# Performance work log

Hardware: AMD Instinct MI355X
Metric: run time of the kernel (lower is better)

Reference implementation:

```python
import jax, jax.numpy as jnp
import numpy as np

# Static config (matches init_kwargs)
N = 1024        # node_num
F = 64          # input_dim (window length)
D = 64          # dim == embed_dim (heads=1)
TOPK = 20
B = 64
EPS = 1e-5      # BatchNorm eps
NEG_SLOPE = 0.2 # GraphLayer leaky_relu slope


def setup_inputs() -> dict:
    key = jax.random.key(0)
    ks = jax.random.split(key, 12)
    s = lambda fan: 1.0 / np.sqrt(fan)
    inp = {
        'data': jax.random.normal(ks[0], (B, N, F), jnp.float32),
        'org_edge_index': jax.random.randint(ks[1], (2, 2048), 0, N),
        'embedding': jax.random.normal(ks[2], (N, D), jnp.float32) * s(D),   # nn.Embedding(node_num, dim), xavier-ish
        'lin_w': jax.random.normal(ks[3], (F, D), jnp.float32) * s(F),       # GraphLayer lin (bias=False)
        'att_i': jax.random.normal(ks[4], (D,), jnp.float32) * s(D),
        'att_j': jax.random.normal(ks[5], (D,), jnp.float32) * s(D),
        'att_em_i': jax.random.normal(ks[6], (D,), jnp.float32) * s(D),
        'att_em_j': jax.random.normal(ks[7], (D,), jnp.float32) * s(D),
        'gnn_bias': jnp.zeros((D,), jnp.float32),
        'bn1_gamma': jnp.ones((D,), jnp.float32),  # GNNLayer.bn
        'bn1_beta': jnp.zeros((D,), jnp.float32),
        'bn2_gamma': jnp.ones((D,), jnp.float32),  # bn_outlayer_in
        'bn2_beta': jnp.zeros((D,), jnp.float32),
        'out_w': jax.random.normal(ks[8], (D, 1), jnp.float32) * s(D),       # OutLayer Linear(dim, 1)
        'out_b': jnp.zeros((1,), jnp.float32),
    }
    return inp


def _batchnorm(x, gamma, beta, axes):
    # training-mode BatchNorm: batch statistics over `axes`, per-feature affine
    mu = jnp.mean(x, axis=axes, keepdims=True)
    var = jnp.var(x, axis=axes, keepdims=True)
    return gamma * (x - mu) * jax.lax.rsqrt(var + EPS) + beta


def reference(data, org_edge_index, embedding, lin_w, att_i, att_j, att_em_i,
              att_em_j, gnn_bias, bn1_gamma, bn1_beta, bn2_gamma, bn2_beta,
              out_w, out_b):
    # --- dynamic graph construction from embedding cosine similarity ---
    w = jax.lax.stop_gradient(embedding)          # weights_arr.detach()
    nrm = jnp.linalg.norm(w, axis=-1)
    cos = (w @ w.T) / jnp.clip(nrm[:, None] * nrm[None, :], 1e-10)
    _, topi = jax.lax.top_k(cos, TOPK)            # [N, TOPK] neighbors j of each target i
    # (torch code drops edges whose cos value is exactly 0 -- measure-zero with
    #  random embeddings; edge count stays N*TOPK. Self edge i->i is always in topk,
    #  matching remove_self_loops + add_self_loops.)

    # --- GraphLayer (GAT-style, heads=1, concat=False, aggr='add') ---
    xl = jnp.einsum('bnf,fd->bnd', data, lin_w)   # linear transform, [B,N,D]
    xj = xl[:, topi]                               # gather neighbor feats [B,N,TOPK,D]
    ej = embedding[topi]                           # neighbor embeddings [N,TOPK,D]
    # alpha = <key_i, att_i||att_em_i> + <key_j, att_j||att_em_j>
    score = (xl @ att_i)[:, :, None] \
          + (embedding @ att_em_i)[None, :, None] \
          + jnp.einsum('bnkd,d->bnk', xj, att_j) \
          + (ej @ att_em_j)[None]                  # [B,N,TOPK]
    alpha = jax.nn.softmax(jax.nn.leaky_relu(score, NEG_SLOPE), axis=-1)
    gnn = jnp.einsum('bnk,bnkd->bnd', alpha, xj) + gnn_bias

    # GNNLayer.bn: BatchNorm1d over B*N samples, D channels
    gnn = _batchnorm(gnn, bn1_gamma, bn1_beta, axes=(0, 1))

    # --- readout ---
    out = gnn * embedding[None]                    # mul with node embedding
    out = jax.nn.relu(_batchnorm(out, bn2_gamma, bn2_beta, axes=(0, 1)))
    # dropout(0.2) -> identity (eval)
    pred = (out @ out_w + out_b).reshape(B, N)     # OutLayer: Linear(D, 1)
    return pred, out
```

## Files before the change

kernel.cpp:

```cpp
#include <hip/hip_runtime.h>

#define NN 1024
#define KK 20
#define BN 65536
#define NEG_SLOPE 0.2f

typedef unsigned short u16;
typedef unsigned int u32;
typedef unsigned long long u64;
typedef __attribute__((ext_vector_type(8))) short bf8;
typedef __attribute__((ext_vector_type(4))) float f32x4;

__device__ __forceinline__ float bf2f(u16 h) {
    return __uint_as_float(((u32)h) << 16);
}
__device__ __forceinline__ u16 f2bf(float f) {
    u32 u = __float_as_uint(f);
    u32 lsb = (u >> 16) & 1u;
    u += 0x7fffu + lsb;
    return (u16)(u >> 16);
}
__device__ __forceinline__ void up2(u32 w, float& a, float& b) {
    a = __uint_as_float(w << 16);
    b = __uint_as_float(w & 0xffff0000u);
}
__device__ __forceinline__ bool is_bf(const void* g1) {
    return *(const u32*)g1 == 0x3F803F80u;
}
template <bool BF>
__device__ __forceinline__ float ldf(const void* p, size_t i) {
    if (BF) return bf2f(((const u16*)p)[i]);
    return ((const float*)p)[i];
}
template <bool BF>
__device__ __forceinline__ void stf(void* p, size_t i, float v) {
    if (BF) ((u16*)p)[i] = f2bf(v);
    else ((float*)p)[i] = v;
}
template <bool BF>
__device__ __forceinline__ void ldf2(const void* p, size_t pairidx, float& a, float& b) {
    if (BF) {
        u32 w = ((const u32*)p)[pairidx];
        up2(w, a, b);
    } else {
        float2 v = ((const float2*)p)[pairidx];
        a = v.x;
        b = v.y;
    }
}

template <bool BF>
__device__ void k1a_body(const void* emb, const void* aei, const void* aej,
                         u16* nwH, u16* nwL, float* e_i, float* e_j, float* stats) {
    __shared__ float sme[4][64], sm2[4][64];
    int tid = threadIdx.x;
    int lane = tid & 63, wave = tid >> 6;
    int n = blockIdx.x * 4 + wave;
    float v = ldf<BF>(emb, n * 64 + lane);
    sme[wave][lane] = v;
    sm2[wave][lane] = v * v;
    float s2 = v * v;
    float si = v * ldf<BF>(aei, lane);
    float sj = v * ldf<BF>(aej, lane);
#pragma unroll
    for (int off = 32; off; off >>= 1) {
        s2 += __shfl_xor(s2, off, 64);
        si += __shfl_xor(si, off, 64);
        sj += __shfl_xor(sj, off, 64);
    }
    float rq = rsqrtf(fmaxf(s2, 1e-20f));
    float x = v * rq;
    u16 h = f2bf(x);
    nwH[n * 64 + lane] = h;
    nwL[n * 64 + lane] = f2bf(x - bf2f(h));
    if (lane == 0) { e_i[n] = si; e_j[n] = sj; }
    __syncthreads();
    if (tid < 64) {
        float u1 = sme[0][tid] + sme[1][tid] + sme[2][tid] + sme[3][tid];
        atomicAdd(&stats[320 + tid], 64.f * u1);
    } else if (tid < 128) {
        int d = tid - 64;
        float u2 = sm2[0][d] + sm2[1][d] + sm2[2][d] + sm2[3][d];
        atomicAdd(&stats[384 + d], 64.f * u2);
    }
}
__global__ __launch_bounds__(256) void k1a_norm(const void* emb, const void* aei, const void* aej,
                                                const void* probe, u16* nwH, u16* nwL,
                                                float* e_i, float* e_j, float* stats) {
    if (is_bf(probe)) k1a_body<true>(emb, aei, aej, nwH, nwL, e_i, e_j, stats);
    else k1a_body<false>(emb, aei, aej, nwH, nwL, e_i, e_j, stats);
}

__global__ __launch_bounds__(256) void k1b_gram(const u16* __restrict__ nwH,
                                                const u16* __restrict__ nwL,
                                                float* __restrict__ G) {
    int tid = threadIdx.x;
    int lane = tid & 63, wave = tid >> 6;
    int c = lane & 15, quad = lane >> 4;
    int rowblk = blockIdx.x >> 4, colblk = blockIdx.x & 15;
    int arow = rowblk * 64 + wave * 16 + c;
    bf8 aH[2], aL[2];
#pragma unroll
    for (int s = 0; s < 2; ++s) {
        aH[s] = *(const bf8*)(nwH + (size_t)arow * 64 + s * 32 + quad * 8);
        aL[s] = *(const bf8*)(nwL + (size_t)arow * 64 + s * 32 + quad * 8);
    }
    f32x4 acc[4] = {{0.f, 0.f, 0.f, 0.f}, {0.f, 0.f, 0.f, 0.f}, {0.f, 0.f, 0.f, 0.f}, {0.f, 0.f, 0.f, 0.f}};
#pragma unroll
    for (int t = 0; t < 4; ++t) {
        int bnode = colblk * 64 + t * 16 + c;
#pragma unroll
        for (int s = 0; s < 2; ++s) {
            bf8 bH = *(const bf8*)(nwH + (size_t)bnode * 64 + s * 32 + quad * 8);
            bf8 bL = *(const bf8*)(nwL + (size_t)bnode * 64 + s * 32 + quad * 8);
            acc[t] = __builtin_amdgcn_mfma_f32_16x16x32_bf16(aH[s], bH, acc[t], 0, 0, 0);
            acc[t] = __builtin_amdgcn_mfma_f32_16x16x32_bf16(aH[s], bL, acc[t], 0, 0, 0);
            acc[t] = __builtin_amdgcn_mfma_f32_16x16x32_bf16(aL[s], bH, acc[t], 0, 0, 0);
        }
    }
#pragma unroll
    for (int t = 0; t < 4; ++t) {
#pragma unroll
        for (int reg = 0; reg < 4; ++reg) {
            int row = rowblk * 64 + wave * 16 + quad * 4 + reg;
            G[(size_t)row * 1024 + colblk * 64 + t * 16 + c] = acc[t][reg];
        }
    }
}

__global__ __launch_bounds__(256) void k1c_select(const float* __restrict__ G, int* __restrict__ topi) {
    int lane = threadIdx.x & 63, wave = threadIdx.x >> 6;
    int n = blockIdx.x * 4 + wave;
    const f32x4* gp = (const f32x4*)(G + (size_t)n * 1024 + lane * 16);
    f32x4 v0 = gp[0], v1 = gp[1], v2 = gp[2], v3 = gp[3];
    float c[16] = {v0.x, v0.y, v0.z, v0.w, v1.x, v1.y, v1.z, v1.w,
                   v2.x, v2.y, v2.z, v2.w, v3.x, v3.y, v3.z, v3.w};
    u32 o[16];
#pragma unroll
    for (int j = 0; j < 16; ++j) {
        u32 u = __float_as_uint(c[j]);
        o[j] = u ^ (u32)(((int)u >> 31) | 0x80000000);
    }
    unsigned mask = 0u;
    int keep = 0;
    for (int r = 0; r < KK; ++r) {
        u32 bo = 0u;
        int bj = 0;
#pragma unroll
        for (int j = 0; j < 16; ++j) {
            bool t = !((mask >> j) & 1u) && o[j] > bo;
            bo = t ? o[j] : bo;
            bj = t ? j : bj;
        }
        u64 key = ((u64)bo << 32) | (u32)(~(u32)(lane * 16 + bj));
#pragma unroll
        for (int off = 32; off; off >>= 1) {
            u64 ok = __shfl_xor((unsigned long long)key, off, 64);
            key = ok > key ? ok : key;
        }
        int bm = (int)((~(u32)key) & 1023u);
        if ((bm >> 4) == lane) mask |= 1u << (bm & 15);
        if (lane == r) keep = bm;
    }
    if (lane < KK) topi[n * KK + lane] = keep;
}

template <bool BF>
__device__ void k2_body(const void* data, const void* lin_w, const void* att_i, const void* att_j,
                        u16* xl, float* a_i, float* a_j) {
    __shared__ u16 Bl[64 * 72];
    __shared__ u16 Ct[64 * 72];
    int tid = threadIdx.x;
    {
        int k = tid >> 2, n0 = (tid & 3) * 16;
        if (BF) {
            const u16* lw = (const u16*)lin_w;
#pragma unroll
            for (int i = 0; i < 16; ++i) Bl[(n0 + i) * 72 + k] = lw[k * 64 + n0 + i];
        } else {
            const float* lw = (const float*)lin_w;
#pragma unroll
            for (int i = 0; i < 16; ++i) Bl[(n0 + i) * 72 + k] = f2bf(lw[k * 64 + n0 + i]);
        }
    }
    __syncthreads();
    int lane = tid & 63, wave = tid >> 6;
    int c = lane & 15, quad = lane >> 4;
    int m0 = blockIdx.x * 64 + wave * 16;
    size_t row = (size_t)(m0 + c);
    f32x4 acc[4] = {{0.f, 0.f, 0.f, 0.f}, {0.f, 0.f, 0.f, 0.f}, {0.f, 0.f, 0.f, 0.f}, {0.f, 0.f, 0.f, 0.f}};
#pragma unroll
    for (int s = 0; s < 2; ++s) {
        bf8 a;
        if (BF) {
            a = *(const bf8*)((const u16*)data + row * 64 + s * 32 + quad * 8);
        } else {
            const float* dp = (const float*)data + row * 64 + s * 32 + quad * 8;
            f32x4 x0 = *(const f32x4*)dp;
            f32x4 x1 = *(const f32x4*)(dp + 4);
            a[0] = (short)f2bf(x0.x); a[1] = (short)f2bf(x0.y);
            a[2] = (short)f2bf(x0.z); a[3] = (short)f2bf(x0.w);
            a[4] = (short)f2bf(x1.x); a[5] = (short)f2bf(x1.y);
            a[6] = (short)f2bf(x1.z); a[7] = (short)f2bf(x1.w);
        }
#pragma unroll
        for (int t = 0; t < 4; ++t) {
            bf8 b = *(const bf8*)&Bl[(t * 16 + c) * 72 + s * 32 + quad * 8];
            acc[t] = __builtin_amdgcn_mfma_f32_16x16x32_bf16(a, b, acc[t], 0, 0, 0);
        }
    }
    float wi[4], wj[4];
#pragma unroll
    for (int t = 0; t < 4; ++t) {
        wi[t] = ldf<BF>(att_i, t * 16 + c);
        wj[t] = ldf<BF>(att_j, t * 16 + c);
    }
    float ai4[4] = {0.f, 0.f, 0.f, 0.f}, aj4[4] = {0.f, 0.f, 0.f, 0.f};
#pragma unroll
    for (int t = 0; t < 4; ++t) {
#pragma unroll
        for (int reg = 0; reg < 4; ++reg) {
            float v = acc[t][reg];
            Ct[(wave * 16 + quad * 4 + reg) * 72 + t * 16 + c] = f2bf(v);
            ai4[reg] += v * wi[t];
            aj4[reg] += v * wj[t];
        }
    }
#pragma unroll
    for (int reg = 0; reg < 4; ++reg) {
#pragma unroll
        for (int off = 1; off < 16; off <<= 1) {
            ai4[reg] += __shfl_xor(ai4[reg], off, 64);
            aj4[reg] += __shfl_xor(aj4[reg], off, 64);
        }
    }
    if (c == 0) {
#pragma unroll
        for (int reg = 0; reg < 4; ++reg) {
            a_i[m0 + quad * 4 + reg] = ai4[reg];
            a_j[m0 + quad * 4 + reg] = aj4[reg];
        }
    }
    __syncthreads();
    {
        int r = tid >> 2, seg = tid & 3;
        uint4 v0 = *(const uint4*)&Ct[r * 72 + seg * 16];
        uint4 v1 = *(const uint4*)&Ct[r * 72 + seg * 16 + 8];
        uint4* dst = (uint4*)xl + ((size_t)(blockIdx.x * 64 + r) * 8 + seg * 2);
        dst[0] = v0;
        dst[1] = v1;
    }
}
__global__ __launch_bounds__(256) void k2_mfma(const void* data, const void* lin_w,
                                               const void* att_i, const void* att_j, const void* probe,
                                               u16* xl, float* a_i, float* a_j) {
    if (is_bf(probe)) k2_body<true>(data, lin_w, att_i, att_j, xl, a_i, a_j);
    else k2_body<false>(data, lin_w, att_i, att_j, xl, a_i, a_j);
}

template <bool BF>
__device__ void k3_body(const u16* xl, const int* topi, const float* a_i, const float* a_j,
                        const float* e_i, const float* e_j, const void* emb,
                        const void* gnn_bias, void* dout, float* stats) {
    extern __shared__ char smem[];
    u32* slice = (u32*)smem;
    float* aje = (float*)(smem + 131072);
    float* aie = (float*)(smem + 135168);
    uint2* sp = (uint2*)(smem + 136192);
    int tid = threadIdx.x;
    int b = blockIdx.x & 63;
    int q = blockIdx.x >> 6;
    int n0 = q * 256;
    const uint4* src = (const uint4*)(xl + ((size_t)b << 16));
    uint4* dst = (uint4*)slice;
#pragma unroll
    for (int r = 0; r < 8; ++r) dst[r * 1024 + tid] = src[r * 1024 + tid];
    aje[tid] = a_j[(b << 10) + tid] + e_j[tid];
    if (tid < 256) aie[tid] = a_i[(b << 10) + n0 + tid] + e_i[n0 + tid];
    __syncthreads();
    int lane = tid & 63, wave = tid >> 6;
    int half = lane >> 5, hl = lane & 31;
    int hwid = wave * 2 + half;
    float bias0, bias1;
    ldf2<BF>(gnn_bias, hl, bias0, bias1);
    float se[10];
#pragma unroll
    for (int s = 0; s < 10; ++s) se[s] = 0.f;
    int nl0 = hwid * 8;
    int t = (hl < KK) ? topi[(n0 + nl0) * KK + hl] : 0;
    for (int ii = 0; ii < 8; ++ii) {
        int nl = nl0 + ii;
        int n = n0 + nl;
        int pair = (b << 10) + n;
        int tc = t;
        if (ii < 7 && hl < KK) t = topi[(n + 1) * KK + hl];
        float sc = -3e38f;
        if (hl < KK) {
            sc = aie[nl] + aje[tc];
            sc = sc >= 0.f ? sc : NEG_SLOPE * sc;
        }
        float m = sc;
#pragma unroll
        for (int off = 16; off; off >>= 1) m = fmaxf(m, __shfl_xor(m, off, 32));
        float p = (hl < KK) ? __expf(sc - m) : 0.f;
        float S = p;
#pragma unroll
        for (int off = 16; off; off >>= 1) S += __shfl_xor(S, off, 32);
        if (hl < KK) {
            uint2 v; v.x = (u32)tc; v.y = __float_as_uint(p / S);
            sp[hwid * KK + hl] = v;
        }
        float acc0 = 0.f, acc1 = 0.f;
#pragma unroll
        for (int k = 0; k < KK; ++k) {
            uint2 v = sp[hwid * KK + k];
            u32 w = slice[(v.x << 5) + hl];
            float alpha = __uint_as_float(v.y);
            acc0 += alpha * __uint_as_float(w << 16);
            acc1 += alpha * __uint_as_float(w & 0xffff0000u);
        }
        acc0 += bias0;
        acc1 += bias1;
        if (BF) {
            u32 pk = (u32)f2bf(acc0) | ((u32)f2bf(acc1) << 16);
            ((u32*)dout)[(BN >> 1) + pair * 32 + hl] = pk;
        } else {
            float2 v2; v2.x = acc0; v2.y = acc1;
            ((float2*)dout)[(BN >> 1) + pair * 32 + hl] = v2;
        }
        float em0, em1;
        ldf2<BF>(emb, n * 32 + hl, em0, em1);
        se[0] += acc0; se[1] += acc1;
        se[2] += acc0 * acc0; se[3] += acc1 * acc1;
        float ge0 = acc0 * em0, ge1 = acc1 * em1;
        se[4] += ge0; se[5] += ge1;
        se[6] += ge0 * ge0; se[7] += ge1 * ge1;
        se[8] += ge0 * em0; se[9] += ge1 * em1;
    }
#pragma unroll
    for (int s = 0; s < 10; ++s) se[s] += __shfl_xor(se[s], 32, 64);
    __syncthreads();
    float* ps = (float*)smem;
    if (half == 0) {
#pragma unroll
        for (int s = 0; s < 5; ++s) {
            ps[wave * 320 + s * 64 + 2 * hl] = se[2 * s];
            ps[wave * 320 + s * 64 + 2 * hl + 1] = se[2 * s + 1];
        }
    }
    __syncthreads();
    if (tid < 320) {
        float s = 0.f;
#pragma unroll
        for (int w = 0; w < 16; ++w) s += ps[w * 320 + tid];
        atomicAdd(&stats[tid], s);
    }
}
__global__ __launch_bounds__(1024) void k3_gnn(const u16* xl, const int* topi, const float* a_i,
                                               const float* a_j, const float* e_i, const float* e_j,
                                               const void* emb, const void* gnn_bias, const void* probe,
                                               void* dout, float* stats) {
    if (is_bf(probe)) k3_body<true>(xl, topi, a_i, a_j, e_i, e_j, emb, gnn_bias, dout, stats);
    else k3_body<false>(xl, topi, a_i, a_j, e_i, e_j, emb, gnn_bias, dout, stats);
}

template <bool BF>
__device__ void k5_body(const void* emb, const float* stats, const void* g1, const void* b1,
                        const void* g2, const void* b2, const void* out_w, const void* out_b,
                        void* dout) {
    int lane = threadIdx.x & 63;
    float P, Q, R;
    {
        int d = lane;
        double inv = 1.0 / 65536.0;
        double S1 = stats[d], S2 = stats[64 + d], T1 = stats[128 + d], T2 = stats[192 + d];
        double T3 = stats[256 + d], U1 = stats[320 + d], U2 = stats[384 + d];
        double mu1 = S1 * inv;
        double var1 = S2 * inv - mu1 * mu1;
        if (var1 < 0.0) var1 = 0.0;
        double r1 = 1.0 / sqrt(var1 + 1e-5);
        double A = (double)ldf<BF>(g1, d) * r1;
        double C = (double)ldf<BF>(b1, d) - A * mu1;
        double E1 = A * T1 + C * U1;
        double mu2 = E1 * inv;
        double E2 = A * A * T2 + 2.0 * A * C * T3 + C * C * U2;
        double var2 = E2 * inv - mu2 * mu2;
        if (var2 < 0.0) var2 = 0.0;
        double r2 = 1.0 / sqrt(var2 + 1e-5);
        double g2r2 = (double)ldf<BF>(g2, d) * r2;
        P = (float)(g2r2 * A);
        Q = (float)(g2r2 * C);
        R = (float)((double)ldf<BF>(b2, d) - g2r2 * mu2);
    }
    int gw = (blockIdx.x * 256 + threadIdx.x) >> 6;
    float wo = ldf<BF>(out_w, lane);
    float ob = ldf<BF>(out_b, 0);
    int row0 = gw * 8;
    for (int i = 0; i < 8; ++i) {
        int row = row0 + i;
        int n = row & 1023;
        size_t oi = (size_t)BN + (size_t)row * 64 + lane;
        float g = ldf<BF>(dout, oi);
        float em = ldf<BF>(emb, n * 64 + lane);
        float o = fmaxf(P * g * em + Q * em + R, 0.f);
        stf<BF>(dout, oi, o);
        float p = o * wo;
#pragma unroll
        for (int off = 32; off; off >>= 1) p += __shfl_xor(p, off, 64);
        if (lane == 0) stf<BF>(dout, row, p + ob);
    }
}
__global__ __launch_bounds__(256) void k5_out(const void* emb, const float* stats, const void* g1,
                                              const void* b1, const void* g2, const void* b2,
                                              const void* out_w, const void* out_b, void* dout) {
    if (is_bf(g1)) k5_body<true>(emb, stats, g1, b1, g2, b2, out_w, out_b, dout);
    else k5_body<false>(emb, stats, g1, b1, g2, b2, out_w, out_b, dout);
}

extern "C" void kernel_launch(void* const* d_in, const int* in_sizes, int n_in,
                              void* d_out, int out_size, void* d_ws, size_t ws_size,
                              hipStream_t stream) {
    const void* data = d_in[0];
    const void* emb = d_in[2];
    const void* lin_w = d_in[3];
    const void* att_i = d_in[4];
    const void* att_j = d_in[5];
    const void* att_em_i = d_in[6];
    const void* att_em_j = d_in[7];
    const void* gnn_bias = d_in[8];
    const void* bn1_g = d_in[9];
    const void* bn1_b = d_in[10];
    const void* bn2_g = d_in[11];
    const void* bn2_b = d_in[12];
    const void* out_w = d_in[13];
    const void* out_b = d_in[14];

    char* ws = (char*)d_ws;
    float* a_i = (float*)ws;
    float* a_j = a_i + 65536;
    float* e_i = a_j + 65536;
    float* e_j = e_i + 1024;
    float* stats = e_j + 1024;
    int* topi = (int*)(stats + 448);
    u16* xl = (u16*)(topi + 20480);
    u16* nwH = xl + 4194304;
    u16* nwL = nwH + 65536;
    float* G = (float*)(nwL + 65536);

    hipMemsetAsync(stats, 0, 448 * sizeof(float), stream);
    k1a_norm<<<256, 256, 0, stream>>>(emb, att_em_i, att_em_j, bn1_g, nwH, nwL, e_i, e_j, stats);
    k1b_gram<<<256, 256, 0, stream>>>(nwH, nwL, G);
    k1c_select<<<256, 256, 0, stream>>>(G, topi);
    k2_mfma<<<1024, 256, 0, stream>>>(data, lin_w, att_i, att_j, bn1_g, xl, a_i, a_j);
    k3_gnn<<<256, 1024, 141312, stream>>>(xl, topi, a_i, a_j, e_i, e_j, emb, gnn_bias, bn1_g,
                                          d_out, stats);
    k5_out<<<2048, 256, 0, stream>>>(emb, stats, bn1_g, bn1_b, bn2_g, bn2_b, out_w, out_b, d_out);
}
```

Baseline: 164.9 us.

## Merge top-k select into xl GEMM launch and software-pipeline attention softmax

```diff
diff --git a/kernel.cpp b/kernel.cpp
--- a/kernel.cpp
+++ b/kernel.cpp
@@ -128,9 +128,9 @@
     }
 }
 
-__global__ __launch_bounds__(256) void k1c_select(const float* __restrict__ G, int* __restrict__ topi) {
+__device__ void k1c_body(int blk, const float* __restrict__ G, int* __restrict__ topi) {
     int lane = threadIdx.x & 63, wave = threadIdx.x >> 6;
-    int n = blockIdx.x * 4 + wave;
+    int n = blk * 4 + wave;
     const f32x4* gp = (const f32x4*)(G + (size_t)n * 1024 + lane * 16);
     f32x4 v0 = gp[0], v1 = gp[1], v2 = gp[2], v3 = gp[3];
     float c[16] = {v0.x, v0.y, v0.z, v0.w, v1.x, v1.y, v1.z, v1.w,
@@ -166,8 +166,8 @@
 }
 
 template <bool BF>
-__device__ void k2_body(const void* data, const void* lin_w, const void* att_i, const void* att_j,
-                        u16* xl, float* a_i, float* a_j) {
+__device__ void k2_body(int blk, const void* data, const void* lin_w, const void* att_i,
+                        const void* att_j, u16* xl, float* a_i, float* a_j) {
     __shared__ u16 Bl[64 * 72];
     __shared__ u16 Ct[64 * 72];
     int tid = threadIdx.x;
@@ -186,7 +186,7 @@
     __syncthreads();
     int lane = tid & 63, wave = tid >> 6;
     int c = lane & 15, quad = lane >> 4;
-    int m0 = blockIdx.x * 64 + wave * 16;
+    int m0 = blk * 64 + wave * 16;
     size_t row = (size_t)(m0 + c);
     f32x4 acc[4] = {{0.f, 0.f, 0.f, 0.f}, {0.f, 0.f, 0.f, 0.f}, {0.f, 0.f, 0.f, 0.f}, {0.f, 0.f, 0.f, 0.f}};
 #pragma unroll
@@ -246,16 +246,22 @@
         int r = tid >> 2, seg = tid & 3;
         uint4 v0 = *(const uint4*)&Ct[r * 72 + seg * 16];
         uint4 v1 = *(const uint4*)&Ct[r * 72 + seg * 16 + 8];
-        uint4* dst = (uint4*)xl + ((size_t)(blockIdx.x * 64 + r) * 8 + seg * 2);
+        uint4* dst = (uint4*)xl + ((size_t)(blk * 64 + r) * 8 + seg * 2);
         dst[0] = v0;
         dst[1] = v1;
     }
 }
-__global__ __launch_bounds__(256) void k2_mfma(const void* data, const void* lin_w,
-                                               const void* att_i, const void* att_j, const void* probe,
-                                               u16* xl, float* a_i, float* a_j) {
-    if (is_bf(probe)) k2_body<true>(data, lin_w, att_i, att_j, xl, a_i, a_j);
-    else k2_body<false>(data, lin_w, att_i, att_j, xl, a_i, a_j);
+
+__global__ __launch_bounds__(256) void k12_fused(const void* data, const void* lin_w,
+                                                 const void* att_i, const void* att_j,
+                                                 const void* probe, u16* xl, float* a_i,
+                                                 float* a_j, const float* G, int* topi) {
+    if (blockIdx.x < 1024) {
+        if (is_bf(probe)) k2_body<true>(blockIdx.x, data, lin_w, att_i, att_j, xl, a_i, a_j);
+        else k2_body<false>(blockIdx.x, data, lin_w, att_i, att_j, xl, a_i, a_j);
+    } else {
+        k1c_body(blockIdx.x - 1024, G, topi);
+    }
 }
 
 template <bool BF>
@@ -287,40 +293,68 @@
 #pragma unroll
     for (int s = 0; s < 10; ++s) se[s] = 0.f;
     int nl0 = hwid * 8;
-    int t = (hl < KK) ? topi[(n0 + nl0) * KK + hl] : 0;
+    u32 tc = 0;
+    float al = 0.f;
+    {
+        int t = (hl < KK) ? topi[(n0 + nl0) * KK + hl] : 0;
+        float sc = -3e38f;
+        if (hl < KK) {
+            sc = aie[nl0] + aje[t];
+            sc = sc >= 0.f ? sc : NEG_SLOPE * sc;
+        }
+        float m = sc;
+#pragma unroll
+        for (int off = 16; off; off >>= 1) m = fmaxf(m, __shfl_xor(m, off, 32));
+        float p = (hl < KK) ? __expf(sc - m) : 0.f;
+        float S = p;
+#pragma unroll
+        for (int off = 16; off; off >>= 1) S += __shfl_xor(S, off, 32);
+        tc = (u32)t;
+        al = p / S;
+    }
     for (int ii = 0; ii < 8; ++ii) {
         int nl = nl0 + ii;
         int n = n0 + nl;
         int pair = (b << 10) + n;
-        int tc = t;
-        if (ii < 7 && hl < KK) t = topi[(n + 1) * KK + hl];
-        float sc = -3e38f;
         if (hl < KK) {
-            sc = aie[nl] + aje[tc];
-            sc = sc >= 0.f ? sc : NEG_SLOPE * sc;
-        }
-        float m = sc;
-#pragma unroll
-        for (int off = 16; off; off >>= 1) m = fmaxf(m, __shfl_xor(m, off, 32));
-        float p = (hl < KK) ? __expf(sc - m) : 0.f;
-        float S = p;
-#pragma unroll
-        for (int off = 16; off; off >>= 1) S += __shfl_xor(S, off, 32);
-        if (hl < KK) {
-            uint2 v; v.x = (u32)tc; v.y = __float_as_uint(p / S);
+            uint2 v; v.x = tc; v.y = __float_as_uint(al);
             sp[hwid * KK + hl] = v;
         }
-        float acc0 = 0.f, acc1 = 0.f;
-#pragma unroll
-        for (int k = 0; k < KK; ++k) {
-            uint2 v = sp[hwid * KK + k];
-            u32 w = slice[(v.x << 5) + hl];
-            float alpha = __uint_as_float(v.y);
-            acc0 += alpha * __uint_as_float(w << 16);
-            acc1 += alpha * __uint_as_float(w & 0xffff0000u);
-        }
-        acc0 += bias0;
-        acc1 += bias1;
+        u32 tn = 0;
+        float aln = 0.f;
+        if (ii < 7) {
+            int t = (hl < KK) ? topi[(n + 1) * KK + hl] : 0;
+            float sc = -3e38f;
+            if (hl < KK) {
+                sc = aie[nl + 1] + aje[t];
+                sc = sc >= 0.f ? sc : NEG_SLOPE * sc;
+            }
+            float m = sc;
+#pragma unroll
+            for (int off = 16; off; off >>= 1) m = fmaxf(m, __shfl_xor(m, off, 32));
+            float p = (hl < KK) ? __expf(sc - m) : 0.f;
+            float S = p;
+#pragma unroll
+            for (int off = 16; off; off >>= 1) S += __shfl_xor(S, off, 32);
+            tn = (u32)t;
+            aln = p / S;
+        }
+        float a0e = 0.f, a0o = 0.f, a1e = 0.f, a1o = 0.f;
+#pragma unroll
+        for (int k = 0; k < KK; k += 2) {
+            uint2 v0 = sp[hwid * KK + k];
+            uint2 v1 = sp[hwid * KK + k + 1];
+            u32 w0 = slice[(v0.x << 5) + hl];
+            u32 w1 = slice[(v1.x << 5) + hl];
+            float p0 = __uint_as_float(v0.y);
+            float p1 = __uint_as_float(v1.y);
+            a0e += p0 * __uint_as_float(w0 << 16);
+            a1e += p0 * __uint_as_float(w0 & 0xffff0000u);
+            a0o += p1 * __uint_as_float(w1 << 16);
+            a1o += p1 * __uint_as_float(w1 & 0xffff0000u);
+        }
+        float acc0 = a0e + a0o + bias0;
+        float acc1 = a1e + a1o + bias1;
         if (BF) {
             u32 pk = (u32)f2bf(acc0) | ((u32)f2bf(acc1) << 16);
             ((u32*)dout)[(BN >> 1) + pair * 32 + hl] = pk;
@@ -336,6 +370,8 @@
         se[4] += ge0; se[5] += ge1;
         se[6] += ge0 * ge0; se[7] += ge1 * ge1;
         se[8] += ge0 * em0; se[9] += ge1 * em1;
+        tc = tn;
+        al = aln;
     }
 #pragma unroll
     for (int s = 0; s < 10; ++s) se[s] += __shfl_xor(se[s], 32, 64);
@@ -450,8 +486,7 @@
     hipMemsetAsync(stats, 0, 448 * sizeof(float), stream);
     k1a_norm<<<256, 256, 0, stream>>>(emb, att_em_i, att_em_j, bn1_g, nwH, nwL, e_i, e_j, stats);
     k1b_gram<<<256, 256, 0, stream>>>(nwH, nwL, G);
-    k1c_select<<<256, 256, 0, stream>>>(G, topi);
-    k2_mfma<<<1024, 256, 0, stream>>>(data, lin_w, att_i, att_j, bn1_g, xl, a_i, a_j);
+    k12_fused<<<1280, 256, 0, stream>>>(data, lin_w, att_i, att_j, bn1_g, xl, a_i, a_j, G, topi);
     k3_gnn<<<256, 1024, 141312, stream>>>(xl, topi, a_i, a_j, e_i, e_j, emb, gnn_bias, bn1_g,
                                           d_out, stats);
     k5_out<<<2048, 256, 0, stream>>>(emb, stats, bn1_g, bn1_b, bn2_g, bn2_b, out_w, out_b, d_out);
```

Result: faster. 161.2 us (-2.2%).
